# Kernel tuning notes

Measured on AMD Instinct MI355X. Metric: run time of the kernel, lower is better.

## Reference

```python
import jax, jax.numpy as jnp
import numpy as np


def setup_inputs() -> dict:
    key = jax.random.key(0)
    k1, k2, k3 = jax.random.split(key, 3)
    B, S, I, H = 32, 1024, 512, 1024
    x = jax.random.normal(k1, (B, S, I), dtype=jnp.float32)
    W_in = jax.random.normal(k2, (I, H), dtype=jnp.float32) * 0.1
    W_rec = jax.random.normal(k3, (H, H), dtype=jnp.float32) * 0.1
    bias = jnp.zeros((H,), dtype=jnp.float32)
    tau = jnp.ones((H,), dtype=jnp.float32) * 0.1
    return {"x": x, "W_in": W_in, "W_rec": W_rec, "bias": bias, "tau": tau}


def reference(x, W_in, W_rec, bias, tau):
    # x: [B, S, I]; liquid / CT-RNN cell with leaky integration.
    B = x.shape[0]
    H = W_rec.shape[0]
    DT = 0.05  # integration step used in the original module
    alpha = jnp.exp(-DT / tau)  # [H], constant across timesteps
    h0 = jnp.zeros((B, H), dtype=x.dtype)
    # Precompute input projection for all steps in one big GEMM: [B,S,H]
    h_in_all = jnp.einsum('bsi,ih->bsh', x, W_in)

    def step(h, h_in_t):
        h_total = jnp.tanh(h_in_t + h @ W_rec + bias)
        h_new = alpha * h + (1.0 - alpha) * h_total
        return h_new, h_new

    # scan over time: xs [S, B, H]
    h_last, outs = jax.lax.scan(step, h0, jnp.swapaxes(h_in_all, 0, 1))
    output = jnp.swapaxes(outs, 0, 1)  # [B, S, H]
    return output, h_last
```

## Files before the change

### kernel.cpp

```cpp
#include <hip/hip_runtime.h>
#include <cmath>

constexpr int B = 32, S = 1024, I = 512, H = 1024;
constexpr float DT = 0.05f;
constexpr unsigned CANARY = 0x40000000u;

__global__ __launch_bounds__(256) void gemm_in(const float* __restrict__ A,
                                               const float* __restrict__ Bw,
                                               float* __restrict__ C) {
    const int bx = blockIdx.x;
    const int nb = bx & 15;
    const int mb = bx >> 4;
    const int t  = threadIdx.x;
    const int tx = t & 15, ty = t >> 4;

    __shared__ __align__(16) float As[16][68];
    __shared__ __align__(16) float Bs[16][68];

    float acc[4][4] = {};
    const int row0 = mb * 64, col0 = nb * 64;

    for (int kt = 0; kt < I; kt += 16) {
        {
            const int m  = t >> 2;
            const int kq = (t & 3) * 4;
            const float4 a = *(const float4*)(A + (size_t)(row0 + m) * I + kt + kq);
            As[kq + 0][m] = a.x; As[kq + 1][m] = a.y;
            As[kq + 2][m] = a.z; As[kq + 3][m] = a.w;
            const int kk = t >> 4;
            const int n4 = (t & 15) * 4;
            *(float4*)&Bs[kk][n4] =
                *(const float4*)(Bw + (size_t)(kt + kk) * H + col0 + n4);
        }
        __syncthreads();
#pragma unroll
        for (int kk = 0; kk < 16; ++kk) {
            const float4 av = *(const float4*)&As[kk][ty * 4];
            const float4 bv = *(const float4*)&Bs[kk][tx * 4];
            const float ar[4] = {av.x, av.y, av.z, av.w};
            const float br[4] = {bv.x, bv.y, bv.z, bv.w};
#pragma unroll
            for (int i = 0; i < 4; ++i)
#pragma unroll
                for (int j = 0; j < 4; ++j) acc[i][j] += ar[i] * br[j];
        }
        __syncthreads();
    }
#pragma unroll
    for (int i = 0; i < 4; ++i) {
        float4 v = make_float4(acc[i][0], acc[i][1], acc[i][2], acc[i][3]);
        *(float4*)(C + (size_t)(row0 + ty * 4 + i) * H + col0 + tx * 4) = v;
    }
}

__device__ __forceinline__ void fma4(float4& acc, float sc, const float4 wv) {
    acc.x = fmaf(sc, wv.x, acc.x);
    acc.y = fmaf(sc, wv.y, acc.y);
    acc.z = fmaf(sc, wv.z, acc.z);
    acc.w = fmaf(sc, wv.w, acc.w);
}

__device__ __forceinline__ void sta(float* p, float v) {
    __hip_atomic_store(p, v, __ATOMIC_RELAXED, __HIP_MEMORY_SCOPE_AGENT);
}
__device__ __forceinline__ unsigned long long ld2(const float* p) {
    return __hip_atomic_load((const unsigned long long*)p, __ATOMIC_RELAXED,
                             __HIP_MEMORY_SCOPE_AGENT);
}
__device__ __forceinline__ void stc(float* p, unsigned v) {
    __hip_atomic_store((unsigned*)p, v, __ATOMIC_RELAXED,
                       __HIP_MEMORY_SCOPE_AGENT);
}
__device__ __forceinline__ float uf(unsigned x) { return __uint_as_float(x); }
__device__ __forceinline__ bool has_canary(unsigned long long q) {
    return ((unsigned)q == CANARY) || ((unsigned)(q >> 32) == CANARY);
}

__global__ __launch_bounds__(256, 1) void scan_k(const float* __restrict__ Wrec,
                                                 const float* __restrict__ bias,
                                                 const float* __restrict__ tau,
                                                 float* __restrict__ out,
                                                 int* __restrict__ ws) {
    const int t    = threadIdx.x;
    const int bid  = blockIdx.x;
    const int rep  = bid & 7;
    const int slot = bid >> 3;
    const int b0   = rep * 4;
    const int c0   = slot * 32;

    __shared__ __align__(16) float h_lds[4 * 1152];
    __shared__ __align__(16) float part[32 * 132];

    int* const flags   = ws;
    int* const myflag  = flags + (((rep << 5) | (t >> 3)) << 5);
    int* const pubflag = flags + (((rep << 5) | slot) << 5);

    const int ks = t >> 3;
    const int cq = t & 7;
    const int cc = c0 + cq * 4;
    float4 wreg[32];
#pragma unroll
    for (int kk = 0; kk < 32; ++kk)
        wreg[kk] = *(const float4*)&Wrec[(size_t)(ks * 32 + kk) * H + cc];

    const int br = t >> 5, jc = t & 31;
    const int c  = c0 + jc;
    float al = 0.f, bi = 0.f;
    if (t < 128) { al = __expf(-DT / tau[c]); bi = bias[c]; }
    const size_t obase = (size_t)(b0 + br) * S * H + c;

    const int wa = 4 * t + (t >> 3) * 4;

    float hinCur = 0.f;
    if (t < 128) hinCur = out[obase];
    __syncthreads();
    if (t < 128) stc(&out[obase], CANARY);
    __syncthreads();
    if (t == 0)
        __hip_atomic_store(pubflag, 1, __ATOMIC_RELAXED,
                           __HIP_MEMORY_SCOPE_AGENT);

    for (int s = 0; s < S; ++s) {
        float hinNext = 0.f;
        if (t < 128 && s + 1 < S) hinNext = out[obase + (size_t)(s + 1) * H];

        if (s == 0) {
            const float4 z = make_float4(0.f, 0.f, 0.f, 0.f);
#pragma unroll
            for (int bb = 0; bb < 4; ++bb)
                *(float4*)&h_lds[bb * 1152 + wa] = z;
        } else {
            if (s == 1) {
                while (__hip_atomic_load(myflag, __ATOMIC_RELAXED,
                                         __HIP_MEMORY_SCOPE_AGENT) < 1)
                    __builtin_amdgcn_s_sleep(1);
            }
            const float* src = out + (size_t)(s - 1) * H + 4 * t;
            const float* p0 = src + (size_t)(b0 + 0) * S * H;
            const float* p1 = src + (size_t)(b0 + 1) * S * H;
            const float* p2 = src + (size_t)(b0 + 2) * S * H;
            const float* p3 = src + (size_t)(b0 + 3) * S * H;
            unsigned long long q0, q1, q2, q3, q4, q5, q6, q7;
            for (;;) {
                q0 = ld2(p0); q1 = ld2(p0 + 2);
                q2 = ld2(p1); q3 = ld2(p1 + 2);
                q4 = ld2(p2); q5 = ld2(p2 + 2);
                q6 = ld2(p3); q7 = ld2(p3 + 2);
                const bool bad = has_canary(q0) | has_canary(q1) |
                                 has_canary(q2) | has_canary(q3) |
                                 has_canary(q4) | has_canary(q5) |
                                 has_canary(q6) | has_canary(q7);
                if (!bad) break;
                __builtin_amdgcn_s_sleep(1);
            }
            const float4 v0 = make_float4(uf((unsigned)q0), uf((unsigned)(q0 >> 32)),
                                          uf((unsigned)q1), uf((unsigned)(q1 >> 32)));
            const float4 v1 = make_float4(uf((unsigned)q2), uf((unsigned)(q2 >> 32)),
                                          uf((unsigned)q3), uf((unsigned)(q3 >> 32)));
            const float4 v2 = make_float4(uf((unsigned)q4), uf((unsigned)(q4 >> 32)),
                                          uf((unsigned)q5), uf((unsigned)(q5 >> 32)));
            const float4 v3 = make_float4(uf((unsigned)q6), uf((unsigned)(q6 >> 32)),
                                          uf((unsigned)q7), uf((unsigned)(q7 >> 32)));
            *(float4*)&h_lds[0 * 1152 + wa] = v0;
            *(float4*)&h_lds[1 * 1152 + wa] = v1;
            *(float4*)&h_lds[2 * 1152 + wa] = v2;
            *(float4*)&h_lds[3 * 1152 + wa] = v3;
        }

        __syncthreads();

        if (t < 128 && s + 1 < S)
            stc(&out[obase + (size_t)(s + 1) * H], CANARY);

        float4 a0 = make_float4(0.f, 0.f, 0.f, 0.f);
        float4 a1 = a0, a2 = a0, a3 = a0;
#pragma unroll
        for (int kq = 0; kq < 8; ++kq) {
            const int ha = ks * 36 + kq * 4;
            const float4 h0 = *(const float4*)&h_lds[ha];
            const float4 h1 = *(const float4*)&h_lds[1152 + ha];
            const float4 h2 = *(const float4*)&h_lds[2304 + ha];
            const float4 h3 = *(const float4*)&h_lds[3456 + ha];
            const float r0[4] = {h0.x, h0.y, h0.z, h0.w};
            const float r1[4] = {h1.x, h1.y, h1.z, h1.w};
            const float r2[4] = {h2.x, h2.y, h2.z, h2.w};
            const float r3[4] = {h3.x, h3.y, h3.z, h3.w};
#pragma unroll
            for (int j = 0; j < 4; ++j) {
                const float4 w = wreg[kq * 4 + j];
                fma4(a0, r0[j], w);
                fma4(a1, r1[j], w);
                fma4(a2, r2[j], w);
                fma4(a3, r3[j], w);
            }
        }
        {
            float* pp = &part[ks * 132 + cq * 4];
            *(float4*)(pp +  0) = a0;
            *(float4*)(pp + 32) = a1;
            *(float4*)(pp + 64) = a2;
            *(float4*)(pp + 96) = a3;
        }
        __syncthreads();

        if (t < 128) {
            float sum = 0.f;
#pragma unroll
            for (int q = 0; q < 32; ++q) sum += part[q * 132 + t];
            const float z  = hinCur + sum + bi;
            const float e2 = __expf(2.f * z);
            const float ht = 1.f - 2.f / (e2 + 1.f);
            const float hp = h_lds[br * 1152 + slot * 36 + jc];
            const float hn = al * hp + (1.f - al) * ht;
            sta(&out[obase + (size_t)s * H], hn);
            if (s == S - 1)
                out[(size_t)B * S * H + (size_t)(b0 + br) * H + c] = hn;
        }
        hinCur = hinNext;
    }
}

extern "C" void kernel_launch(void* const* d_in, const int* in_sizes, int n_in,
                              void* d_out, int out_size, void* d_ws, size_t ws_size,
                              hipStream_t stream) {
    (void)in_sizes; (void)n_in; (void)out_size;
    const float* x    = (const float*)d_in[0];
    const float* W_in = (const float*)d_in[1];
    const float* Wrec = (const float*)d_in[2];
    const float* bs   = (const float*)d_in[3];
    const float* tu   = (const float*)d_in[4];
    float* outp = (float*)d_out;
    int*   bwsp = (int*)d_ws;

    size_t zb = 256 * 32 * sizeof(int);
    if (zb > ws_size) zb = ws_size;
    (void)hipMemsetAsync(d_ws, 0, zb, stream);

    gemm_in<<<dim3(512 * 16), dim3(256), 0, stream>>>(x, W_in, outp);

    void* kargs[5] = {(void*)&Wrec, (void*)&bs, (void*)&tu, (void*)&outp,
                      (void*)&bwsp};
    (void)hipLaunchCooperativeKernel((void*)scan_k, dim3(256), dim3(256), kargs,
                                     0, stream);
}
```

Measured before the change: 3.436 ms.

## Double the scan block to 512 threads and drop a per-step barrier

The recurrent scan kernel now launches 512 threads per block. Each thread holds float2 slices of W_rec instead of float4, halving per-thread FMA work and register pressure. The barrier between filling h_lds and the matvec is removed, which relies on each thread group reading only h values written within its own wavefront. The partial-sum buffer is double-buffered so the next step can start without a second barrier. The canary check now masks the sign bit and the canary keeps the sign of the prefetched input value. The risk is subtle cross-wave races on the shared buffers in exchange for less synchronisation per timestep.

```diff
diff --git a/kernel.cpp b/kernel.cpp
--- a/kernel.cpp
+++ b/kernel.cpp
@@ -53,11 +53,9 @@
     }
 }
 
-__device__ __forceinline__ void fma4(float4& acc, float sc, const float4 wv) {
+__device__ __forceinline__ void fma2(float2& acc, float sc, const float2 wv) {
     acc.x = fmaf(sc, wv.x, acc.x);
     acc.y = fmaf(sc, wv.y, acc.y);
-    acc.z = fmaf(sc, wv.z, acc.z);
-    acc.w = fmaf(sc, wv.w, acc.w);
 }
 
 __device__ __forceinline__ void sta(float* p, float v) {
@@ -73,10 +71,11 @@
 }
 __device__ __forceinline__ float uf(unsigned x) { return __uint_as_float(x); }
 __device__ __forceinline__ bool has_canary(unsigned long long q) {
-    return ((unsigned)q == CANARY) || ((unsigned)(q >> 32) == CANARY);
-}
-
-__global__ __launch_bounds__(256, 1) void scan_k(const float* __restrict__ Wrec,
+    return (((unsigned)q & 0x7FFFFFFFu) == CANARY) ||
+           (((unsigned)(q >> 32) & 0x7FFFFFFFu) == CANARY);
+}
+
+__global__ __launch_bounds__(512, 1) void scan_k(const float* __restrict__ Wrec,
                                                  const float* __restrict__ bias,
                                                  const float* __restrict__ tau,
                                                  float* __restrict__ out,
@@ -88,20 +87,21 @@
     const int b0   = rep * 4;
     const int c0   = slot * 32;
 
+    const int ks  = t >> 4;
+    const int cq2 = t & 15;
+
     __shared__ __align__(16) float h_lds[4 * 1152];
-    __shared__ __align__(16) float part[32 * 132];
+    __shared__ __align__(16) float part[2][32 * 132];
 
     int* const flags   = ws;
-    int* const myflag  = flags + (((rep << 5) | (t >> 3)) << 5);
+    int* const myflag  = flags + (((rep << 5) | ks) << 5);
     int* const pubflag = flags + (((rep << 5) | slot) << 5);
 
-    const int ks = t >> 3;
-    const int cq = t & 7;
-    const int cc = c0 + cq * 4;
-    float4 wreg[32];
+    const int cc = c0 + cq2 * 2;
+    float2 wreg[32];
 #pragma unroll
     for (int kk = 0; kk < 32; ++kk)
-        wreg[kk] = *(const float4*)&Wrec[(size_t)(ks * 32 + kk) * H + cc];
+        wreg[kk] = *(const float2*)&Wrec[(size_t)(ks * 32 + kk) * H + cc];
 
     const int br = t >> 5, jc = t & 31;
     const int c  = c0 + jc;
@@ -109,7 +109,7 @@
     if (t < 128) { al = __expf(-DT / tau[c]); bi = bias[c]; }
     const size_t obase = (size_t)(b0 + br) * S * H + c;
 
-    const int wa = 4 * t + (t >> 3) * 4;
+    const int wa2 = 2 * t + ks * 4;
 
     float hinCur = 0.f;
     if (t < 128) hinCur = out[obase];
@@ -125,55 +125,47 @@
         if (t < 128 && s + 1 < S) hinNext = out[obase + (size_t)(s + 1) * H];
 
         if (s == 0) {
-            const float4 z = make_float4(0.f, 0.f, 0.f, 0.f);
+            const float2 z = make_float2(0.f, 0.f);
 #pragma unroll
             for (int bb = 0; bb < 4; ++bb)
-                *(float4*)&h_lds[bb * 1152 + wa] = z;
+                *(float2*)&h_lds[bb * 1152 + wa2] = z;
         } else {
             if (s == 1) {
                 while (__hip_atomic_load(myflag, __ATOMIC_RELAXED,
                                          __HIP_MEMORY_SCOPE_AGENT) < 1)
                     __builtin_amdgcn_s_sleep(1);
             }
-            const float* src = out + (size_t)(s - 1) * H + 4 * t;
+            const float* src = out + (size_t)(s - 1) * H + 2 * t;
             const float* p0 = src + (size_t)(b0 + 0) * S * H;
             const float* p1 = src + (size_t)(b0 + 1) * S * H;
             const float* p2 = src + (size_t)(b0 + 2) * S * H;
             const float* p3 = src + (size_t)(b0 + 3) * S * H;
-            unsigned long long q0, q1, q2, q3, q4, q5, q6, q7;
+            unsigned long long q0, q1, q2, q3;
             for (;;) {
-                q0 = ld2(p0); q1 = ld2(p0 + 2);
-                q2 = ld2(p1); q3 = ld2(p1 + 2);
-                q4 = ld2(p2); q5 = ld2(p2 + 2);
-                q6 = ld2(p3); q7 = ld2(p3 + 2);
+                q0 = ld2(p0); q1 = ld2(p1); q2 = ld2(p2); q3 = ld2(p3);
                 const bool bad = has_canary(q0) | has_canary(q1) |
-                                 has_canary(q2) | has_canary(q3) |
-                                 has_canary(q4) | has_canary(q5) |
-                                 has_canary(q6) | has_canary(q7);
+                                 has_canary(q2) | has_canary(q3);
                 if (!bad) break;
                 __builtin_amdgcn_s_sleep(1);
             }
-            const float4 v0 = make_float4(uf((unsigned)q0), uf((unsigned)(q0 >> 32)),
-                                          uf((unsigned)q1), uf((unsigned)(q1 >> 32)));
-            const float4 v1 = make_float4(uf((unsigned)q2), uf((unsigned)(q2 >> 32)),
-                                          uf((unsigned)q3), uf((unsigned)(q3 >> 32)));
-            const float4 v2 = make_float4(uf((unsigned)q4), uf((unsigned)(q4 >> 32)),
-                                          uf((unsigned)q5), uf((unsigned)(q5 >> 32)));
-            const float4 v3 = make_float4(uf((unsigned)q6), uf((unsigned)(q6 >> 32)),
-                                          uf((unsigned)q7), uf((unsigned)(q7 >> 32)));
-            *(float4*)&h_lds[0 * 1152 + wa] = v0;
-            *(float4*)&h_lds[1 * 1152 + wa] = v1;
-            *(float4*)&h_lds[2 * 1152 + wa] = v2;
-            *(float4*)&h_lds[3 * 1152 + wa] = v3;
-        }
-
-        __syncthreads();
-
-        if (t < 128 && s + 1 < S)
-            stc(&out[obase + (size_t)(s + 1) * H], CANARY);
-
-        float4 a0 = make_float4(0.f, 0.f, 0.f, 0.f);
-        float4 a1 = a0, a2 = a0, a3 = a0;
+            *(float2*)&h_lds[0 * 1152 + wa2] =
+                make_float2(uf((unsigned)q0), uf((unsigned)(q0 >> 32)));
+            *(float2*)&h_lds[1 * 1152 + wa2] =
+                make_float2(uf((unsigned)q1), uf((unsigned)(q1 >> 32)));
+            *(float2*)&h_lds[2 * 1152 + wa2] =
+                make_float2(uf((unsigned)q2), uf((unsigned)(q2 >> 32)));
+            *(float2*)&h_lds[3 * 1152 + wa2] =
+                make_float2(uf((unsigned)q3), uf((unsigned)(q3 >> 32)));
+        }
+
+        if (t < 128 && s + 1 < S) {
+            const unsigned cb =
+                CANARY | (__float_as_uint(hinNext) & 0x80000000u);
+            stc(&out[obase + (size_t)(s + 1) * H], cb);
+        }
+
+        float2 a0 = make_float2(0.f, 0.f);
+        float2 a1 = a0, a2 = a0, a3 = a0;
 #pragma unroll
         for (int kq = 0; kq < 8; ++kq) {
             const int ha = ks * 36 + kq * 4;
@@ -187,26 +179,27 @@
             const float r3[4] = {h3.x, h3.y, h3.z, h3.w};
 #pragma unroll
             for (int j = 0; j < 4; ++j) {
-                const float4 w = wreg[kq * 4 + j];
-                fma4(a0, r0[j], w);
-                fma4(a1, r1[j], w);
-                fma4(a2, r2[j], w);
-                fma4(a3, r3[j], w);
+                const float2 w = wreg[kq * 4 + j];
+                fma2(a0, r0[j], w);
+                fma2(a1, r1[j], w);
+                fma2(a2, r2[j], w);
+                fma2(a3, r3[j], w);
             }
         }
         {
-            float* pp = &part[ks * 132 + cq * 4];
-            *(float4*)(pp +  0) = a0;
-            *(float4*)(pp + 32) = a1;
-            *(float4*)(pp + 64) = a2;
-            *(float4*)(pp + 96) = a3;
+            float* pp = &part[s & 1][ks * 132 + cq2 * 2];
+            *(float2*)(pp +  0) = a0;
+            *(float2*)(pp + 32) = a1;
+            *(float2*)(pp + 64) = a2;
+            *(float2*)(pp + 96) = a3;
         }
         __syncthreads();
 
         if (t < 128) {
+            const float* pb = &part[s & 1][0];
             float sum = 0.f;
 #pragma unroll
-            for (int q = 0; q < 32; ++q) sum += part[q * 132 + t];
+            for (int q = 0; q < 32; ++q) sum += pb[q * 132 + t];
             const float z  = hinCur + sum + bi;
             const float e2 = __expf(2.f * z);
             const float ht = 1.f - 2.f / (e2 + 1.f);
@@ -240,6 +233,6 @@
 
     void* kargs[5] = {(void*)&Wrec, (void*)&bs, (void*)&tu, (void*)&outp,
                       (void*)&bwsp};
-    (void)hipLaunchCooperativeKernel((void*)scan_k, dim3(256), dim3(256), kargs,
+    (void)hipLaunchCooperativeKernel((void*)scan_k, dim3(256), dim3(512), kargs,
                                      0, stream);
 }
```

After: 3.329 ms. 1.03x faster.
